# Kernel optimization log

Hardware: AMD Instinct MI355X
Metric: run time of the kernel (lower is better)

## Reference

```python
import jax, jax.numpy as jnp
import numpy as np

B, S, D = 4, 2048, 2048
NQ, NKV = 16, 4
HD = D // NQ          # head_size = 128
GROUP = NQ // NKV     # 4


def _rope_table(seq_len, head_size, theta=10000.0):
    # [seq, head_size/2, 2] = (cos, sin), matching torch polar freqs_cis
    inv = 1.0 / (theta ** (np.arange(0, head_size, 2, dtype=np.float32) / head_size))
    ang = np.arange(seq_len, dtype=np.float32)[:, None] * inv[None, :]
    return jnp.asarray(np.stack([np.cos(ang), np.sin(ang)], axis=-1))


def setup_inputs() -> dict:
    key = jax.random.key(0)
    ks = jax.random.split(key, 6)
    sd = 0.02
    return {
        "x": jax.random.normal(ks[0], (B, S, D), jnp.float32),
        "freq_cis": _rope_table(S, HD),
        "Wq": jax.random.normal(ks[1], (D, NQ * HD), jnp.float32) * sd,
        "bq": jnp.zeros((NQ * HD,), jnp.float32),
        "Wk": jax.random.normal(ks[2], (D, NKV * HD), jnp.float32) * sd,
        "bk": jnp.zeros((NKV * HD,), jnp.float32),
        "Wv": jax.random.normal(ks[3], (D, NKV * HD), jnp.float32) * sd,
        "bv": jnp.zeros((NKV * HD,), jnp.float32),
        "Wo": jax.random.normal(ks[4], (NQ * HD, D), jnp.float32) * sd,
        "start_pos": 0,
    }


def _apply_rope(x, fc):
    # x: [b, s, h, d]; fc: [s, d/2, 2] -> complex multiply on (even, odd) pairs
    xr = x.reshape(*x.shape[:-1], -1, 2)
    cos = fc[None, :, None, :, 0]
    sin = fc[None, :, None, :, 1]
    x0, x1 = xr[..., 0], xr[..., 1]
    out = jnp.stack([x0 * cos - x1 * sin, x0 * sin + x1 * cos], axis=-1)
    return out.reshape(x.shape)


def reference(x, freq_cis, Wq, bq, Wk, bk, Wv, bv, Wo, start_pos):
    b, s, _ = x.shape
    q = (x @ Wq + bq).reshape(b, s, NQ, HD)
    k = (x @ Wk + bk).reshape(b, s, NKV, HD)
    v = (x @ Wv + bv).reshape(b, s, NKV, HD)

    fc = freq_cis[start_pos:start_pos + s]
    q = _apply_rope(q, fc)
    k = _apply_rope(k, fc)

    # [b, nkv, group, s, d] query view; k/v stay [b, nkv, s, d] (GQA broadcast)
    q = q.transpose(0, 2, 1, 3).reshape(b, NKV, GROUP, s, HD)
    k = k.transpose(0, 2, 1, 3)
    v = v.transpose(0, 2, 1, 3)

    scale = 1.0 / jnp.sqrt(jnp.asarray(HD, x.dtype))
    scores = jnp.einsum("bhgqd,bhkd->bhgqk", q, k) * scale
    causal = jnp.tril(jnp.ones((s, s), bool))
    scores = jnp.where(causal[None, None, None], scores, jnp.asarray(-jnp.inf, scores.dtype))
    probs = jax.nn.softmax(scores, axis=-1)
    o = jnp.einsum("bhgqk,bhkd->bhgqd", probs, v)

    o = o.reshape(b, NQ, s, HD).transpose(0, 2, 1, 3).reshape(b, s, NQ * HD)
    return o @ Wo
```

## Files before the change

kernel.cpp:

```cpp
#include <hip/hip_runtime.h>
#include <stdint.h>

typedef __attribute__((ext_vector_type(8))) short bf16x8;
typedef __attribute__((ext_vector_type(4))) float f32x4;
typedef __attribute__((ext_vector_type(16))) float f32x16;

#define S_LEN 2048
#define D_MODEL 2048
#define NQH 16
#define NKVH 4
#define HDIM 128
#define BATCH 4

__device__ __forceinline__ float bf2f(unsigned short s) {
  union { unsigned u; float f; } v; v.u = ((unsigned)s) << 16; return v.f;
}
__device__ __forceinline__ unsigned short f2bf(float f) {
  union { float f; unsigned u; } v; v.f = f;
  unsigned r = v.u + 0x7FFFu + ((v.u >> 16) & 1u);
  return (unsigned short)(r >> 16);
}
__device__ __forceinline__ f32x4 fzero() {
  f32x4 v; v[0]=0.f; v[1]=0.f; v[2]=0.f; v[3]=0.f; return v;
}
__device__ __forceinline__ void async16(const void* g, void* l) {
  __builtin_amdgcn_global_load_lds(
      (const __attribute__((address_space(1))) unsigned int*)g,
      (__attribute__((address_space(3))) unsigned int*)l, 16, 0, 0);
}
__device__ __forceinline__ unsigned cvtpk(float lo, float hi) {
  unsigned r;
  asm("v_cvt_pk_bf16_f32 %0, %1, %2" : "=v"(r) : "v"(lo), "v"(hi));
  return r;
}

__global__ void k_convert_x(const float* __restrict__ x, unsigned short* __restrict__ xb, int n4) {
  int stride = gridDim.x * blockDim.x;
  for (int i = blockIdx.x * blockDim.x + threadIdx.x; i < n4; i += stride) {
    float4 v = ((const float4*)x)[i];
    ushort4 o;
    o.x = f2bf(v.x); o.y = f2bf(v.y); o.z = f2bf(v.z); o.w = f2bf(v.w);
    ((ushort4*)xb)[i] = o;
  }
}

__global__ void k_transpose_all(const float* __restrict__ Wq, const float* __restrict__ Wk,
                                const float* __restrict__ Wv, const float* __restrict__ Wo,
                                unsigned short* __restrict__ Wt, unsigned short* __restrict__ Wot) {
  __shared__ float tile[32][33];
  int bid = blockIdx.x;
  const float* W; unsigned short* D; int N, nx;
  if (bid < 4096)      { W = Wq; D = Wt;                          N = 2048; nx = 64; }
  else if (bid < 5120) { W = Wk; D = Wt + (size_t)2048 * 2048;    N = 512;  nx = 16; bid -= 4096; }
  else if (bid < 6144) { W = Wv; D = Wt + (size_t)2560 * 2048;    N = 512;  nx = 16; bid -= 5120; }
  else                 { W = Wo; D = Wot;                         N = 2048; nx = 64; bid -= 6144; }
  int tx = threadIdx.x & 31, ty = threadIdx.x >> 5;
  int n0 = (bid % nx) * 32, k0 = (bid / nx) * 32;
  #pragma unroll
  for (int i = 0; i < 4; ++i)
    tile[ty + i*8][tx] = W[(size_t)(k0 + ty + i*8) * N + n0 + tx];
  __syncthreads();
  #pragma unroll
  for (int i = 0; i < 4; ++i)
    D[(size_t)(n0 + ty + i*8) * 2048 + k0 + tx] = f2bf(tile[tx][ty + i*8]);
}

__global__ void k_ropeK(unsigned short* __restrict__ Kb, const float* __restrict__ fc,
                        const int* __restrict__ start_pos, int total) {
  int sp = start_pos[0];
  int stride = gridDim.x * blockDim.x;
  for (int i = blockIdx.x * blockDim.x + threadIdx.x; i < total; i += stride) {
    int d2 = i & 63;
    int s = (i >> 6) & (S_LEN - 1);
    unsigned v = ((unsigned*)Kb)[i];
    float x0 = bf2f((unsigned short)(v & 0xFFFFu));
    float x1 = bf2f((unsigned short)(v >> 16));
    float c  = fc[((size_t)(sp + s) * 64 + d2) * 2];
    float sn = fc[((size_t)(sp + s) * 64 + d2) * 2 + 1];
    float y0 = x0 * c - x1 * sn;
    float y1 = x0 * sn + x1 * c;
    ((unsigned*)Kb)[i] = (unsigned)f2bf(y0) | ((unsigned)f2bf(y1) << 16);
  }
}

#define BARRIER() __builtin_amdgcn_s_barrier()
#define LGKM0()  do { asm volatile("s_waitcnt lgkmcnt(0)" ::: "memory"); \
                      __builtin_amdgcn_sched_barrier(0); } while (0)
#define VMCNT6() asm volatile("s_waitcnt vmcnt(6)" ::: "memory")
#define VMCNT4() asm volatile("s_waitcnt vmcnt(4)" ::: "memory")
#define VMCNT0() asm volatile("s_waitcnt vmcnt(0)" ::: "memory")

__device__ __forceinline__ bf16x8 ldsrd(const unsigned short* L, int row, int kk, int g) {
  int Xs = (kk * 64 + g * 16) ^ ((row & 7) << 4);
  return *(const bf16x8*)&L[row * 64 + (Xs >> 1)];
}
__device__ __forceinline__ void stage8(const unsigned short* __restrict__ G, int gbase,
                                       int k0, unsigned short* lds, int rowbase, int lane) {
  int row = rowbase + (lane >> 3);
  int col8 = (lane & 7) ^ ((lane >> 3) & 7);
  async16(G + (size_t)(gbase + row) * 2048 + k0 + col8 * 8, lds + rowbase * 64 + lane * 8);
}

const float SCL2E_H = 0.08838834764831845f * 1.4426950408889634f;

__global__ __launch_bounds__(512, 2) void k_gemm_q(
    const unsigned short* __restrict__ A, const unsigned short* __restrict__ Bt,
    const float* __restrict__ bq, unsigned short* __restrict__ Qo)
{
  __shared__ __align__(16) unsigned short Abuf[2][256 * 64];
  __shared__ __align__(16) unsigned short Bbuf[2][256 * 64];
  const int NT = 32, NXT = 8;
  const int tid = threadIdx.x, lane = tid & 63, w = tid >> 6;
  const int lr = lane & 15, g = lane >> 4;
  const int wm = w >> 2, wn = w & 3;

  int nwg = NXT * 32;
  int cpx = nwg >> 3;
  int bid = blockIdx.x;
  int swz = (bid & 7) * cpx + (bid >> 3);
  const int by = swz / NXT, bx = swz % NXT;
  const int mbase = by * 256, nbase = bx * 256;

  #define ST_AQ02(tt) if ((tt) < NT) { unsigned short* L = Abuf[(tt) & 1]; int k0 = (tt) * 64; \
    _Pragma("unroll") for (int it = 0; it < 2; ++it) { int sub = it * 8 + w; \
      stage8(A, mbase, k0, L, (sub >> 3) * 128 + (sub & 7) * 8, lane); } }
  #define ST_AQ13(tt) if ((tt) < NT) { unsigned short* L = Abuf[(tt) & 1]; int k0 = (tt) * 64; \
    _Pragma("unroll") for (int it = 0; it < 2; ++it) { int sub = it * 8 + w; \
      stage8(A, mbase, k0, L, 64 + (sub >> 3) * 128 + (sub & 7) * 8, lane); } }
  #define ST_BS0(tt) if ((tt) < NT) { unsigned short* L = Bbuf[(tt) & 1]; int k0 = (tt) * 64; \
    _Pragma("unroll") for (int it = 0; it < 2; ++it) { int sub = it * 8 + w; \
      stage8(Bt, nbase, k0, L, (sub >> 2) * 64 + (sub & 3) * 8, lane); } }
  #define ST_BS1(tt) if ((tt) < NT) { unsigned short* L = Bbuf[(tt) & 1]; int k0 = (tt) * 64; \
    _Pragma("unroll") for (int it = 0; it < 2; ++it) { int sub = it * 8 + w; \
      stage8(Bt, nbase, k0, L, 32 + (sub >> 2) * 64 + (sub & 3) * 8, lane); } }

  f32x4 acc[8][4];
  #pragma unroll
  for (int m = 0; m < 8; ++m)
    #pragma unroll
    for (int n = 0; n < 4; ++n) acc[m][n] = fzero();

  ST_AQ02(0); ST_AQ13(0); ST_BS0(0); ST_BS1(0);
  ST_AQ02(1); ST_BS1(1);
  VMCNT4();
  BARRIER();

  bf16x8 a[2][4], b[2][2];

  for (int t = 0; t < NT; ++t) {
    const unsigned short* Al = Abuf[t & 1];
    const unsigned short* Bl = Bbuf[t & 1];

    #pragma unroll
    for (int kk = 0; kk < 2; ++kk) {
      #pragma unroll
      for (int m = 0; m < 4; ++m) a[kk][m] = ldsrd(Al, wm * 128 + m * 16 + lr, kk, g);
      #pragma unroll
      for (int n = 0; n < 2; ++n) b[kk][n] = ldsrd(Bl, wn * 64 + n * 16 + lr, kk, g);
    }
    ST_AQ13(t + 1);
    BARRIER(); LGKM0();
    __builtin_amdgcn_s_setprio(1);
    #pragma unroll
    for (int kk = 0; kk < 2; ++kk)
      #pragma unroll
      for (int m = 0; m < 4; ++m)
        #pragma unroll
        for (int n = 0; n < 2; ++n)
          acc[m][n] = __builtin_amdgcn_mfma_f32_16x16x32_bf16(a[kk][m], b[kk][n], acc[m][n], 0, 0, 0);
    __builtin_amdgcn_s_setprio(0);
    BARRIER();

    #pragma unroll
    for (int kk = 0; kk < 2; ++kk)
      #pragma unroll
      for (int n = 0; n < 2; ++n) b[kk][n] = ldsrd(Bl, wn * 64 + (2 + n) * 16 + lr, kk, g);
    ST_BS0(t + 1);
    BARRIER(); LGKM0();
    __builtin_amdgcn_s_setprio(1);
    #pragma unroll
    for (int kk = 0; kk < 2; ++kk)
      #pragma unroll
      for (int m = 0; m < 4; ++m)
        #pragma unroll
        for (int n = 0; n < 2; ++n)
          acc[m][2 + n] = __builtin_amdgcn_mfma_f32_16x16x32_bf16(a[kk][m], b[kk][n], acc[m][2 + n], 0, 0, 0);
    __builtin_amdgcn_s_setprio(0);
    BARRIER();

    #pragma unroll
    for (int kk = 0; kk < 2; ++kk)
      #pragma unroll
      for (int m = 0; m < 4; ++m) a[kk][m] = ldsrd(Al, wm * 128 + 64 + m * 16 + lr, kk, g);
    ST_AQ02(t + 2);
    BARRIER(); LGKM0();
    __builtin_amdgcn_s_setprio(1);
    #pragma unroll
    for (int kk = 0; kk < 2; ++kk)
      #pragma unroll
      for (int m = 0; m < 4; ++m)
        #pragma unroll
        for (int n = 0; n < 2; ++n)
          acc[4 + m][2 + n] = __builtin_amdgcn_mfma_f32_16x16x32_bf16(a[kk][m], b[kk][n], acc[4 + m][2 + n], 0, 0, 0);
    __builtin_amdgcn_s_setprio(0);
    BARRIER();

    #pragma unroll
    for (int kk = 0; kk < 2; ++kk)
      #pragma unroll
      for (int n = 0; n < 2; ++n) b[kk][n] = ldsrd(Bl, wn * 64 + n * 16 + lr, kk, g);
    ST_BS1(t + 2);
    VMCNT4();
    BARRIER(); LGKM0();
    __builtin_amdgcn_s_setprio(1);
    #pragma unroll
    for (int kk = 0; kk < 2; ++kk)
      #pragma unroll
      for (int m = 0; m < 4; ++m)
        #pragma unroll
        for (int n = 0; n < 2; ++n)
          acc[4 + m][n] = __builtin_amdgcn_mfma_f32_16x16x32_bf16(a[kk][m], b[kk][n], acc[4 + m][n], 0, 0, 0);
    __builtin_amdgcn_s_setprio(0);
    BARRIER();
  }

  #pragma unroll
  for (int n = 0; n < 4; ++n) {
    const int ng = nbase + wn * 64 + n * 16 + lr;
    const int hh = ng >> 7, dd = ng & 127;
    const float bias = bq[ng];
    #pragma unroll
    for (int m = 0; m < 8; ++m)
      #pragma unroll
      for (int i = 0; i < 4; ++i) {
        int mg = mbase + wm * 128 + m * 16 + g * 4 + i;
        int bb = mg >> 11, s = mg & 2047;
        float val = (acc[m][n][i] + bias) * SCL2E_H;
        Qo[((size_t)(bb * NQH + hh) * S_LEN + s) * HDIM + dd] = f2bf(val);
      }
  }
  #undef ST_AQ02
  #undef ST_AQ13
  #undef ST_BS0
  #undef ST_BS1
}

__global__ __launch_bounds__(512, 2) void k_gemm_kv(
    const unsigned short* __restrict__ A, const unsigned short* __restrict__ Bt,
    const float* __restrict__ bk, const float* __restrict__ bv,
    unsigned short* __restrict__ Ko, unsigned short* __restrict__ Vto)
{
  __shared__ __align__(16) unsigned short Ab[3][256 * 64];
  __shared__ __align__(16) unsigned short Bb[3][128 * 64];
  const int NT = 32, NXT = 8;
  const int tid = threadIdx.x, lane = tid & 63, w = tid >> 6;
  const int lr = lane & 15, g = lane >> 4;
  const int wm = w >> 1, wn = w & 1;

  int nwg = NXT * 32;
  int cpx = nwg >> 3;
  int bid = blockIdx.x;
  int swz = (bid & 7) * cpx + (bid >> 3);
  const int by = swz / NXT, bx = swz % NXT;
  const int mbase = by * 256, nbase = bx * 128;

  #define ST_A(tt) { unsigned short* L = Ab[(tt) % 3]; int k0 = (tt) * 64; \
    _Pragma("unroll") for (int it = 0; it < 4; ++it) { int c = tid + it * 512; \
      int row = c >> 3, col8 = (c & 7) ^ (row & 7); \
      async16(A + (size_t)(mbase + row) * 2048 + k0 + col8 * 8, L + c * 8); } }
  #define ST_B(tt) { unsigned short* L = Bb[(tt) % 3]; int k0 = (tt) * 64; \
    _Pragma("unroll") for (int it = 0; it < 2; ++it) { int c = tid + it * 512; \
      int row = c >> 3, col8 = (c & 7) ^ (row & 7); \
      async16(Bt + (size_t)(nbase + row) * 2048 + k0 + col8 * 8, L + c * 8); } }

  f32x4 acc[4][4];
  #pragma unroll
  for (int m = 0; m < 4; ++m)
    #pragma unroll
    for (int n = 0; n < 4; ++n) acc[m][n] = fzero();

  ST_A(0); ST_B(0); ST_A(1); ST_B(1);
  VMCNT6();
  BARRIER();

  for (int t = 0; t < NT; ++t) {
    const unsigned short* Al = Ab[t % 3];
    const unsigned short* Bl = Bb[t % 3];
    bf16x8 a[2][4], b[2][2];

    #pragma unroll
    for (int kk = 0; kk < 2; ++kk) {
      #pragma unroll
      for (int m = 0; m < 4; ++m) a[kk][m] = ldsrd(Al, wm * 64 + m * 16 + lr, kk, g);
      #pragma unroll
      for (int n = 0; n < 2; ++n) b[kk][n] = ldsrd(Bl, wn * 64 + n * 16 + lr, kk, g);
    }
    if (t + 2 < NT) ST_A(t + 2);
    BARRIER(); LGKM0();
    __builtin_amdgcn_s_setprio(1);
    #pragma unroll
    for (int kk = 0; kk < 2; ++kk)
      #pragma unroll
      for (int m = 0; m < 4; ++m)
        #pragma unroll
        for (int n = 0; n < 2; ++n)
          acc[m][n] = __builtin_amdgcn_mfma_f32_16x16x32_bf16(a[kk][m], b[kk][n], acc[m][n], 0, 0, 0);
    __builtin_amdgcn_s_setprio(0);
    BARRIER();

    #pragma unroll
    for (int kk = 0; kk < 2; ++kk)
      #pragma unroll
      for (int n = 0; n < 2; ++n) b[kk][n] = ldsrd(Bl, wn * 64 + (2 + n) * 16 + lr, kk, g);
    if (t + 2 < NT) { ST_B(t + 2); VMCNT6(); } else { VMCNT0(); }
    BARRIER(); LGKM0();
    __builtin_amdgcn_s_setprio(1);
    #pragma unroll
    for (int kk = 0; kk < 2; ++kk)
      #pragma unroll
      for (int m = 0; m < 4; ++m)
        #pragma unroll
        for (int n = 0; n < 2; ++n)
          acc[m][2 + n] = __builtin_amdgcn_mfma_f32_16x16x32_bf16(a[kk][m], b[kk][n], acc[m][2 + n], 0, 0, 0);
    __builtin_amdgcn_s_setprio(0);
    BARRIER();
  }

  #pragma unroll
  for (int n = 0; n < 4; ++n) {
    const int ng = nbase + wn * 64 + n * 16 + lr;
    const bool isK = (ng < 512);
    const int nn = isK ? ng : ng - 512;
    const int hh = nn >> 7, dd = nn & 127;
    const float bias = isK ? bk[nn] : bv[nn];
    #pragma unroll
    for (int m = 0; m < 4; ++m)
      #pragma unroll
      for (int i = 0; i < 4; ++i) {
        int mg = mbase + wm * 64 + m * 16 + g * 4 + i;
        int bb = mg >> 11, s = mg & 2047;
        float val = acc[m][n][i] + bias;
        if (isK) {
          Ko[((size_t)(bb * NKVH + hh) * S_LEN + s) * HDIM + dd] = f2bf(val);
        } else {
          Vto[((size_t)(bb * NKVH + hh) * HDIM + dd) * S_LEN + s] = f2bf(val);
        }
      }
  }
  #undef ST_A
  #undef ST_B
}

__global__ __launch_bounds__(512, 2) void k_gemm_out256(
    const unsigned short* __restrict__ A, const unsigned short* __restrict__ Bt,
    float* __restrict__ Cf)
{
  __shared__ __align__(16) unsigned short Abuf[2][256 * 64];
  __shared__ __align__(16) unsigned short Bbuf[2][256 * 64];
  const int NT = 32, NXT = 8;
  const int tid = threadIdx.x, lane = tid & 63, w = tid >> 6;
  const int lr = lane & 15, g = lane >> 4;
  const int wm = w >> 2, wn = w & 3;

  int nwg = NXT * 32;
  int cpx = nwg >> 3;
  int bid = blockIdx.x;
  int swz = (bid & 7) * cpx + (bid >> 3);
  const int by = swz / NXT, bx = swz % NXT;
  const int mbase = by * 256, nbase = bx * 256;

  #define ST_AQ02(tt) if ((tt) < NT) { unsigned short* L = Abuf[(tt) & 1]; int k0 = (tt) * 64; \
    _Pragma("unroll") for (int it = 0; it < 2; ++it) { int sub = it * 8 + w; \
      stage8(A, mbase, k0, L, (sub >> 3) * 128 + (sub & 7) * 8, lane); } }
  #define ST_AQ13(tt) if ((tt) < NT) { unsigned short* L = Abuf[(tt) & 1]; int k0 = (tt) * 64; \
    _Pragma("unroll") for (int it = 0; it < 2; ++it) { int sub = it * 8 + w; \
      stage8(A, mbase, k0, L, 64 + (sub >> 3) * 128 + (sub & 7) * 8, lane); } }
  #define ST_BS0(tt) if ((tt) < NT) { unsigned short* L = Bbuf[(tt) & 1]; int k0 = (tt) * 64; \
    _Pragma("unroll") for (int it = 0; it < 2; ++it) { int sub = it * 8 + w; \
      stage8(Bt, nbase, k0, L, (sub >> 2) * 64 + (sub & 3) * 8, lane); } }
  #define ST_BS1(tt) if ((tt) < NT) { unsigned short* L = Bbuf[(tt) & 1]; int k0 = (tt) * 64; \
    _Pragma("unroll") for (int it = 0; it < 2; ++it) { int sub = it * 8 + w; \
      stage8(Bt, nbase, k0, L, 32 + (sub >> 2) * 64 + (sub & 3) * 8, lane); } }

  f32x4 acc[8][4];
  #pragma unroll
  for (int m = 0; m < 8; ++m)
    #pragma unroll
    for (int n = 0; n < 4; ++n) acc[m][n] = fzero();

  ST_AQ02(0); ST_AQ13(0); ST_BS0(0); ST_BS1(0);
  ST_AQ02(1); ST_BS1(1);
  VMCNT4();
  BARRIER();

  bf16x8 a[2][4], b[2][2];

  for (int t = 0; t < NT; ++t) {
    const unsigned short* Al = Abuf[t & 1];
    const unsigned short* Bl = Bbuf[t & 1];

    #pragma unroll
    for (int kk = 0; kk < 2; ++kk) {
      #pragma unroll
      for (int m = 0; m < 4; ++m) a[kk][m] = ldsrd(Al, wm * 128 + m * 16 + lr, kk, g);
      #pragma unroll
      for (int n = 0; n < 2; ++n) b[kk][n] = ldsrd(Bl, wn * 64 + n * 16 + lr, kk, g);
    }
    ST_AQ13(t + 1);
    BARRIER(); LGKM0();
    __builtin_amdgcn_s_setprio(1);
    #pragma unroll
    for (int kk = 0; kk < 2; ++kk)
      #pragma unroll
      for (int m = 0; m < 4; ++m)
        #pragma unroll
        for (int n = 0; n < 2; ++n)
          acc[m][n] = __builtin_amdgcn_mfma_f32_16x16x32_bf16(a[kk][m], b[kk][n], acc[m][n], 0, 0, 0);
    __builtin_amdgcn_s_setprio(0);
    BARRIER();

    #pragma unroll
    for (int kk = 0; kk < 2; ++kk)
      #pragma unroll
      for (int n = 0; n < 2; ++n) b[kk][n] = ldsrd(Bl, wn * 64 + (2 + n) * 16 + lr, kk, g);
    ST_BS0(t + 1);
    BARRIER(); LGKM0();
    __builtin_amdgcn_s_setprio(1);
    #pragma unroll
    for (int kk = 0; kk < 2; ++kk)
      #pragma unroll
      for (int m = 0; m < 4; ++m)
        #pragma unroll
        for (int n = 0; n < 2; ++n)
          acc[m][2 + n] = __builtin_amdgcn_mfma_f32_16x16x32_bf16(a[kk][m], b[kk][n], acc[m][2 + n], 0, 0, 0);
    __builtin_amdgcn_s_setprio(0);
    BARRIER();

    #pragma unroll
    for (int kk = 0; kk < 2; ++kk)
      #pragma unroll
      for (int m = 0; m < 4; ++m) a[kk][m] = ldsrd(Al, wm * 128 + 64 + m * 16 + lr, kk, g);
    ST_AQ02(t + 2);
    BARRIER(); LGKM0();
    __builtin_amdgcn_s_setprio(1);
    #pragma unroll
    for (int kk = 0; kk < 2; ++kk)
      #pragma unroll
      for (int m = 0; m < 4; ++m)
        #pragma unroll
        for (int n = 0; n < 2; ++n)
          acc[4 + m][2 + n] = __builtin_amdgcn_mfma_f32_16x16x32_bf16(a[kk][m], b[kk][n], acc[4 + m][2 + n], 0, 0, 0);
    __builtin_amdgcn_s_setprio(0);
    BARRIER();

    #pragma unroll
    for (int kk = 0; kk < 2; ++kk)
      #pragma unroll
      for (int n = 0; n < 2; ++n) b[kk][n] = ldsrd(Bl, wn * 64 + n * 16 + lr, kk, g);
    ST_BS1(t + 2);
    VMCNT4();
    BARRIER(); LGKM0();
    __builtin_amdgcn_s_setprio(1);
    #pragma unroll
    for (int kk = 0; kk < 2; ++kk)
      #pragma unroll
      for (int m = 0; m < 4; ++m)
        #pragma unroll
        for (int n = 0; n < 2; ++n)
          acc[4 + m][n] = __builtin_amdgcn_mfma_f32_16x16x32_bf16(a[kk][m], b[kk][n], acc[4 + m][n], 0, 0, 0);
    __builtin_amdgcn_s_setprio(0);
    BARRIER();
  }

  #pragma unroll
  for (int m = 0; m < 8; ++m)
    #pragma unroll
    for (int n = 0; n < 4; ++n)
      #pragma unroll
      for (int i = 0; i < 4; ++i) {
        int mg = mbase + wm * 128 + m * 16 + g * 4 + i;
        int ng = nbase + wn * 64 + n * 16 + lr;
        Cf[(size_t)mg * 2048 + ng] = acc[m][n][i];
      }
  #undef ST_AQ02
  #undef ST_AQ13
  #undef ST_BS0
  #undef ST_BS1
}

__global__ __launch_bounds__(256, 2) void k_flash2(
    const unsigned short* __restrict__ Q, const unsigned short* __restrict__ K,
    const unsigned short* __restrict__ Vt, unsigned short* __restrict__ O,
    const float* __restrict__ fc, const int* __restrict__ start_pos)
{
  __shared__ __align__(16) unsigned short SH[32768];

  const int tid = threadIdx.x;
  const int lane = tid & 63;
  const int w = tid >> 6;
  const int ql = lane & 31;
  const int hi = lane >> 5;

  const int bh = blockIdx.x >> 3;
  const int tp = blockIdx.x & 7;
  const int b = bh >> 4, h = bh & 15;
  const int kh = h >> 2;
  const int sp = start_pos[0];

  const unsigned short* Qbase = Q + (size_t)(b * NQH + h) * S_LEN * HDIM;
  const unsigned short* Kbase = K + (size_t)(b * NKVH + kh) * S_LEN * HDIM;
  const unsigned short* Vtb   = Vt + (size_t)(b * NKVH + kh) * HDIM * S_LEN;

  #define STAGEKV(jj) { unsigned short* Kd = SH + ((jj) & 1) * 16384; \
    unsigned short* Vd = Kd + 8192; \
    _Pragma("unroll") for (int it = 0; it < 4; ++it) { \
      int c = tid + it * 256; int row = c >> 4, col = c & 15; \
      int lcol = col ^ (row & 15); \
      async16(Kbase + (size_t)((jj) * 64 + row) * HDIM + lcol * 8, Kd + c * 8); } \
    _Pragma("unroll") for (int it = 0; it < 4; ++it) { \
      int c = tid + it * 256; int row = c >> 3, col = c & 7; \
      int lcol = col ^ (row & 7); \
      async16(Vtb + (size_t)row * S_LEN + (jj) * 64 + lcol * 8, Vd + c * 8); } }

  #pragma unroll 1
  for (int half = 0; half < 2; ++half) {
    const int t = half ? (15 - tp) : tp;
    const int nkv = 2 * t + 2;
    const int qg = t * 128 + w * 32 + ql;

    __syncthreads();

    bf16x8 qf[8];
    {
      const unsigned short* qp = Qbase + (size_t)qg * HDIM;
      const float* fcrow = fc + (size_t)(sp + qg) * 128;
      #pragma unroll
      for (int dd = 0; dd < 8; ++dd) {
        bf16x8 raw = *(const bf16x8*)(qp + dd * 16 + hi * 8);
        int d2b = (dd * 16 + hi * 8) >> 1;
        union { unsigned u[4]; bf16x8 v; } out;
        #pragma unroll
        for (int u2 = 0; u2 < 4; ++u2) {
          float x0 = bf2f((unsigned short)raw[2 * u2]);
          float x1 = bf2f((unsigned short)raw[2 * u2 + 1]);
          float2 cs = *(const float2*)&fcrow[(d2b + u2) * 2];
          out.u[u2] = cvtpk(x0 * cs.x - x1 * cs.y, x0 * cs.y + x1 * cs.x);
        }
        qf[dd] = out.v;
      }
    }

    float m_r = -1e30f, l_r = 0.f;
    f32x16 oA[4];
    #pragma unroll
    for (int db = 0; db < 4; ++db)
      #pragma unroll
      for (int r = 0; r < 16; ++r) oA[db][r] = 0.f;

    STAGEKV(0);
    __syncthreads();

    for (int j = 0; j < nkv; ++j) {
      const unsigned short* Kl = SH + (j & 1) * 16384;
      const unsigned short* Vl = Kl + 8192;

      if (j + 1 < nkv) STAGEKV(j + 1);

      if (j * 64 <= t * 128 + w * 32 + 31) {
        f32x16 p0, p1;
        #pragma unroll
        for (int r = 0; r < 16; ++r) { p0[r] = 0.f; p1[r] = 0.f; }
        __builtin_amdgcn_s_setprio(1);
        #pragma unroll
        for (int dd = 0; dd < 8; ++dd) {
          const int off = (((dd * 32 + hi * 16) ^ ((ql & 15) << 4)) >> 1);
          bf16x8 a0 = *(const bf16x8*)&Kl[ql * 128 + off];
          bf16x8 a1 = *(const bf16x8*)&Kl[(32 + ql) * 128 + off];
          p0 = __builtin_amdgcn_mfma_f32_32x32x16_bf16(a0, qf[dd], p0, 0, 0, 0);
          p1 = __builtin_amdgcn_mfma_f32_32x32x16_bf16(a1, qf[dd], p1, 0, 0, 0);
        }
        __builtin_amdgcn_s_setprio(0);

        #pragma unroll
        for (int r = 0; r < 16; ++r) {
          const int kl = (r & 3) + 8 * (r >> 2);
          int kg = j * 64 + kl + 4 * hi;
          if (kg > qg) p0[r] = -1e30f;
          if (kg + 32 > qg) p1[r] = -1e30f;
        }

        float pm = -1e30f;
        #pragma unroll
        for (int r = 0; r < 16; ++r) pm = fmaxf(pm, fmaxf(p0[r], p1[r]));
        pm = fmaxf(pm, __shfl_xor(pm, 32));
        if (!__all(pm - m_r <= 8.0f)) {
          const float mn = fmaxf(m_r, pm);
          const float corr = exp2f(m_r - mn);
          m_r = mn;
          l_r *= corr;
          #pragma unroll
          for (int db = 0; db < 4; ++db)
            #pragma unroll
            for (int r = 0; r < 16; ++r) oA[db][r] *= corr;
        }
        float rs = 0.f;
        #pragma unroll
        for (int r = 0; r < 16; ++r) {
          p0[r] = exp2f(p0[r] - m_r);
          p1[r] = exp2f(p1[r] - m_r);
          rs += p0[r] + p1[r];
        }
        rs += __shfl_xor(rs, 32);
        l_r += rs;

        bf16x8 pb[4];
        {
          unsigned Wv[8], W2v[8];
          #pragma unroll
          for (int d = 0; d < 4; ++d) {
            Wv[d]      = cvtpk(p0[4*d],     p0[4*d + 1]);
            W2v[d]     = cvtpk(p0[4*d + 2], p0[4*d + 3]);
            Wv[4 + d]  = cvtpk(p1[4*d],     p1[4*d + 1]);
            W2v[4 + d] = cvtpk(p1[4*d + 2], p1[4*d + 3]);
          }
          #pragma unroll
          for (int kt = 0; kt < 2; ++kt) {
            #pragma unroll
            for (int s = 0; s < 2; ++s) {
              unsigned ownW   = hi ? Wv[kt*4 + 2*s + 1]  : Wv[kt*4 + 2*s];
              unsigned sendW  = hi ? Wv[kt*4 + 2*s]      : Wv[kt*4 + 2*s + 1];
              unsigned recvW  = (unsigned)__shfl_xor((int)sendW, 32);
              unsigned ownW2  = hi ? W2v[kt*4 + 2*s + 1] : W2v[kt*4 + 2*s];
              unsigned sendW2 = hi ? W2v[kt*4 + 2*s]     : W2v[kt*4 + 2*s + 1];
              unsigned recvW2 = (unsigned)__shfl_xor((int)sendW2, 32);
              union { unsigned u[4]; bf16x8 v; } pk;
              pk.u[0] = hi ? recvW  : ownW;
              pk.u[1] = hi ? recvW2 : ownW2;
              pk.u[2] = hi ? ownW   : recvW;
              pk.u[3] = hi ? ownW2  : recvW2;
              pb[kt*2 + s] = pk.v;
            }
          }
        }

        __builtin_amdgcn_s_setprio(1);
        #pragma unroll
        for (int ks = 0; ks < 4; ++ks) {
          #pragma unroll
          for (int db = 0; db < 4; ++db) {
            const int off = (((ks * 32 + hi * 16) ^ ((ql & 7) << 4)) >> 1);
            bf16x8 av = *(const bf16x8*)&Vl[(db * 32 + ql) * 64 + off];
            oA[db] = __builtin_amdgcn_mfma_f32_32x32x16_bf16(av, pb[ks], oA[db], 0, 0, 0);
          }
        }
        __builtin_amdgcn_s_setprio(0);
      }
      __syncthreads();
    }

    {
      const float invl = 1.f / l_r;
      const int qloc = w * 32 + ql;
      #pragma unroll
      for (int db = 0; db < 4; ++db)
        #pragma unroll
        for (int g4 = 0; g4 < 4; ++g4) {
          unsigned lo  = cvtpk(oA[db][g4*4 + 0] * invl, oA[db][g4*4 + 1] * invl);
          unsigned hi2 = cvtpk(oA[db][g4*4 + 2] * invl, oA[db][g4*4 + 3] * invl);
          int byteoff = qloc * 256 + ((db * 64 + g4 * 16 + hi * 8) ^ ((qloc & 7) << 4));
          *(uint2*)((char*)SH + byteoff) = make_uint2(lo, hi2);
        }
    }
    __syncthreads();
    {
      const int q2 = tid >> 1, hf = tid & 1;
      unsigned short* orow = O + ((size_t)(b * S_LEN + t * 128 + q2)) * D_MODEL + h * HDIM + hf * 64;
      #pragma unroll
      for (int u = 0; u < 8; ++u) {
        int byteoff = q2 * 256 + ((hf * 128 + u * 16) ^ ((q2 & 7) << 4));
        bf16x8 v = *(const bf16x8*)((const char*)SH + byteoff);
        *(bf16x8*)(orow + u * 8) = v;
      }
    }
  }
  #undef STAGEKV
}

extern "C" void kernel_launch(void* const* d_in, const int* in_sizes, int n_in,
                              void* d_out, int out_size, void* d_ws, size_t ws_size,
                              hipStream_t stream) {
  (void)in_sizes; (void)n_in; (void)out_size; (void)ws_size;
  const float* x  = (const float*)d_in[0];
  const float* fc = (const float*)d_in[1];
  const float* Wq = (const float*)d_in[2];
  const float* bq = (const float*)d_in[3];
  const float* Wk = (const float*)d_in[4];
  const float* bk = (const float*)d_in[5];
  const float* Wv = (const float*)d_in[6];
  const float* bv = (const float*)d_in[7];
  const float* Wo = (const float*)d_in[8];
  const int* start_pos = (const int*)d_in[9];
  float* out = (float*)d_out;

  unsigned short* ws = (unsigned short*)d_ws;
  size_t off = 0;
  unsigned short* xb  = ws + off; off += (size_t)8192 * 2048;
  unsigned short* Wt  = ws + off; off += (size_t)3072 * 2048;
  unsigned short* Wot = ws + off; off += (size_t)2048 * 2048;
  unsigned short* Qb  = ws + off; off += (size_t)BATCH * NQH  * S_LEN * HDIM;
  unsigned short* Kb  = ws + off; off += (size_t)BATCH * NKVH * S_LEN * HDIM;
  unsigned short* Vtb = ws + off; off += (size_t)BATCH * NKVH * S_LEN * HDIM;
  unsigned short* Ob  = ws + off; off += (size_t)8192 * 2048;

  k_convert_x<<<2048, 256, 0, stream>>>(x, xb, 8192 * 2048 / 4);
  k_transpose_all<<<10240, 256, 0, stream>>>(Wq, Wk, Wv, Wo, Wt, Wot);

  k_gemm_q<<<dim3(256), 512, 0, stream>>>(xb, Wt, bq, Qb);
  k_gemm_kv<<<dim3(256), 512, 0, stream>>>(xb, Wt + (size_t)2048 * 2048, bk, bv, Kb, Vtb);

  k_ropeK<<<512, 256, 0, stream>>>(Kb, fc, start_pos, BATCH * NKVH * S_LEN * 64);

  k_flash2<<<dim3(512), 256, 0, stream>>>(Qb, Kb, Vtb, Ob, fc, start_pos);

  k_gemm_out256<<<dim3(256), 512, 0, stream>>>(Ob, Wot, out);
}
```

Before: 362.6 us.

## Shrink flash attention KV tile to 32 and launch one block per query tile

The attention kernel now stages 32-key K/V tiles instead of 64, which halves shared memory and raises launch bounds to 4 blocks per CU. It drops the paired-tile (t, 15-t) load balancing and launches 1024 blocks, one per 128-query tile. The causal mask is applied only on the diagonal tile per wave, and tile skipping is done at 32-key granularity. The cost is more loop iterations and barriers, lower MFMA work per sync, and load balance that now relies on the hardware scheduler instead of explicit pairing.

```diff
diff --git a/kernel.cpp b/kernel.cpp
--- a/kernel.cpp
+++ b/kernel.cpp
@@ -488,12 +488,12 @@
   #undef ST_BS1
 }
 
-__global__ __launch_bounds__(256, 2) void k_flash2(
+__global__ __launch_bounds__(256, 4) void k_flash2(
     const unsigned short* __restrict__ Q, const unsigned short* __restrict__ K,
     const unsigned short* __restrict__ Vt, unsigned short* __restrict__ O,
     const float* __restrict__ fc, const int* __restrict__ start_pos)
 {
-  __shared__ __align__(16) unsigned short SH[32768];
+  __shared__ __align__(16) unsigned short SH[16384];
 
   const int tid = threadIdx.x;
   const int lane = tid & 63;
@@ -501,8 +501,8 @@
   const int ql = lane & 31;
   const int hi = lane >> 5;
 
-  const int bh = blockIdx.x >> 3;
-  const int tp = blockIdx.x & 7;
+  const int bh = blockIdx.x >> 4;
+  const int t  = blockIdx.x & 15;
   const int b = bh >> 4, h = bh & 15;
   const int kh = h >> 2;
   const int sp = start_pos[0];
@@ -511,176 +511,163 @@
   const unsigned short* Kbase = K + (size_t)(b * NKVH + kh) * S_LEN * HDIM;
   const unsigned short* Vtb   = Vt + (size_t)(b * NKVH + kh) * HDIM * S_LEN;
 
-  #define STAGEKV(jj) { unsigned short* Kd = SH + ((jj) & 1) * 16384; \
-    unsigned short* Vd = Kd + 8192; \
-    _Pragma("unroll") for (int it = 0; it < 4; ++it) { \
+  #define STAGEKV(jj) { unsigned short* Kd = SH + ((jj) & 1) * 8192; \
+    unsigned short* Vd = Kd + 4096; \
+    _Pragma("unroll") for (int it = 0; it < 2; ++it) { \
       int c = tid + it * 256; int row = c >> 4, col = c & 15; \
-      int lcol = col ^ (row & 15); \
-      async16(Kbase + (size_t)((jj) * 64 + row) * HDIM + lcol * 8, Kd + c * 8); } \
-    _Pragma("unroll") for (int it = 0; it < 4; ++it) { \
-      int c = tid + it * 256; int row = c >> 3, col = c & 7; \
-      int lcol = col ^ (row & 7); \
-      async16(Vtb + (size_t)row * S_LEN + (jj) * 64 + lcol * 8, Vd + c * 8); } }
-
-  #pragma unroll 1
-  for (int half = 0; half < 2; ++half) {
-    const int t = half ? (15 - tp) : tp;
-    const int nkv = 2 * t + 2;
-    const int qg = t * 128 + w * 32 + ql;
-
-    __syncthreads();
-
-    bf16x8 qf[8];
-    {
-      const unsigned short* qp = Qbase + (size_t)qg * HDIM;
-      const float* fcrow = fc + (size_t)(sp + qg) * 128;
+      int lcol = (col & 8) | ((col ^ (row & 7)) & 7); \
+      async16(Kbase + (size_t)((jj) * 32 + row) * HDIM + lcol * 8, Kd + c * 8); } \
+    _Pragma("unroll") for (int it = 0; it < 2; ++it) { \
+      int c = tid + it * 256; int row = c >> 2, col = c & 3; \
+      int lcol = col ^ (row & 3); \
+      async16(Vtb + (size_t)row * S_LEN + (jj) * 32 + lcol * 8, Vd + c * 8); } }
+
+  const int nkv = 4 * t + 4;
+  const int qg = t * 128 + w * 32 + ql;
+  const int jd = 4 * t + w;
+
+  bf16x8 qf[8];
+  {
+    const unsigned short* qp = Qbase + (size_t)qg * HDIM;
+    const float* fcrow = fc + (size_t)(sp + qg) * 128;
+    #pragma unroll
+    for (int dd = 0; dd < 8; ++dd) {
+      bf16x8 raw = *(const bf16x8*)(qp + dd * 16 + hi * 8);
+      int d2b = (dd * 16 + hi * 8) >> 1;
+      union { unsigned u[4]; bf16x8 v; } out;
+      #pragma unroll
+      for (int u2 = 0; u2 < 4; ++u2) {
+        float x0 = bf2f((unsigned short)raw[2 * u2]);
+        float x1 = bf2f((unsigned short)raw[2 * u2 + 1]);
+        float2 cs = *(const float2*)&fcrow[(d2b + u2) * 2];
+        out.u[u2] = cvtpk(x0 * cs.x - x1 * cs.y, x0 * cs.y + x1 * cs.x);
+      }
+      qf[dd] = out.v;
+    }
+  }
+
+  float m_r = -1e30f, l_r = 0.f;
+  f32x16 oA[4];
+  #pragma unroll
+  for (int db = 0; db < 4; ++db)
+    #pragma unroll
+    for (int r = 0; r < 16; ++r) oA[db][r] = 0.f;
+
+  STAGEKV(0);
+  __syncthreads();
+
+  for (int j = 0; j < nkv; ++j) {
+    const unsigned short* Kl = SH + (j & 1) * 8192;
+    const unsigned short* Vl = Kl + 4096;
+
+    if (j + 1 < nkv) STAGEKV(j + 1);
+
+    if (j <= jd) {
+      f32x16 p0;
+      #pragma unroll
+      for (int r = 0; r < 16; ++r) p0[r] = 0.f;
+      __builtin_amdgcn_s_setprio(1);
       #pragma unroll
       for (int dd = 0; dd < 8; ++dd) {
-        bf16x8 raw = *(const bf16x8*)(qp + dd * 16 + hi * 8);
-        int d2b = (dd * 16 + hi * 8) >> 1;
-        union { unsigned u[4]; bf16x8 v; } out;
-        #pragma unroll
-        for (int u2 = 0; u2 < 4; ++u2) {
-          float x0 = bf2f((unsigned short)raw[2 * u2]);
-          float x1 = bf2f((unsigned short)raw[2 * u2 + 1]);
-          float2 cs = *(const float2*)&fcrow[(d2b + u2) * 2];
-          out.u[u2] = cvtpk(x0 * cs.x - x1 * cs.y, x0 * cs.y + x1 * cs.x);
+        const int off = (((dd * 32 + hi * 16) ^ ((ql & 7) << 4)) >> 1);
+        bf16x8 a0 = *(const bf16x8*)&Kl[ql * 128 + off];
+        p0 = __builtin_amdgcn_mfma_f32_32x32x16_bf16(a0, qf[dd], p0, 0, 0, 0);
+      }
+      __builtin_amdgcn_s_setprio(0);
+
+      if (j == jd) {
+        #pragma unroll
+        for (int r = 0; r < 16; ++r) {
+          const int kl = (r & 3) + 8 * (r >> 2) + 4 * hi;
+          if (kl > ql) p0[r] = -1e30f;
         }
-        qf[dd] = out.v;
-      }
-    }
-
-    float m_r = -1e30f, l_r = 0.f;
-    f32x16 oA[4];
-    #pragma unroll
-    for (int db = 0; db < 4; ++db)
-      #pragma unroll
-      for (int r = 0; r < 16; ++r) oA[db][r] = 0.f;
-
-    STAGEKV(0);
-    __syncthreads();
-
-    for (int j = 0; j < nkv; ++j) {
-      const unsigned short* Kl = SH + (j & 1) * 16384;
-      const unsigned short* Vl = Kl + 8192;
-
-      if (j + 1 < nkv) STAGEKV(j + 1);
-
-      if (j * 64 <= t * 128 + w * 32 + 31) {
-        f32x16 p0, p1;
-        #pragma unroll
-        for (int r = 0; r < 16; ++r) { p0[r] = 0.f; p1[r] = 0.f; }
-        __builtin_amdgcn_s_setprio(1);
-        #pragma unroll
-        for (int dd = 0; dd < 8; ++dd) {
-          const int off = (((dd * 32 + hi * 16) ^ ((ql & 15) << 4)) >> 1);
-          bf16x8 a0 = *(const bf16x8*)&Kl[ql * 128 + off];
-          bf16x8 a1 = *(const bf16x8*)&Kl[(32 + ql) * 128 + off];
-          p0 = __builtin_amdgcn_mfma_f32_32x32x16_bf16(a0, qf[dd], p0, 0, 0, 0);
-          p1 = __builtin_amdgcn_mfma_f32_32x32x16_bf16(a1, qf[dd], p1, 0, 0, 0);
+      }
+
+      float pm = -1e30f;
+      #pragma unroll
+      for (int r = 0; r < 16; ++r) pm = fmaxf(pm, p0[r]);
+      pm = fmaxf(pm, __shfl_xor(pm, 32));
+      if (!__all(pm - m_r <= 8.0f)) {
+        const float mn = fmaxf(m_r, pm);
+        const float corr = exp2f(m_r - mn);
+        m_r = mn;
+        l_r *= corr;
+        #pragma unroll
+        for (int db = 0; db < 4; ++db)
+          #pragma unroll
+          for (int r = 0; r < 16; ++r) oA[db][r] *= corr;
+      }
+      float rs = 0.f;
+      #pragma unroll
+      for (int r = 0; r < 16; ++r) {
+        p0[r] = exp2f(p0[r] - m_r);
+        rs += p0[r];
+      }
+      rs += __shfl_xor(rs, 32);
+      l_r += rs;
+
+      bf16x8 pb[2];
+      {
+        unsigned Wv[4], W2v[4];
+        #pragma unroll
+        for (int d = 0; d < 4; ++d) {
+          Wv[d]  = cvtpk(p0[4*d],     p0[4*d + 1]);
+          W2v[d] = cvtpk(p0[4*d + 2], p0[4*d + 3]);
         }
-        __builtin_amdgcn_s_setprio(0);
-
-        #pragma unroll
-        for (int r = 0; r < 16; ++r) {
-          const int kl = (r & 3) + 8 * (r >> 2);
-          int kg = j * 64 + kl + 4 * hi;
-          if (kg > qg) p0[r] = -1e30f;
-          if (kg + 32 > qg) p1[r] = -1e30f;
+        #pragma unroll
+        for (int s = 0; s < 2; ++s) {
+          unsigned ownW   = hi ? Wv[2*s + 1]  : Wv[2*s];
+          unsigned sendW  = hi ? Wv[2*s]      : Wv[2*s + 1];
+          unsigned recvW  = (unsigned)__shfl_xor((int)sendW, 32);
+          unsigned ownW2  = hi ? W2v[2*s + 1] : W2v[2*s];
+          unsigned sendW2 = hi ? W2v[2*s]     : W2v[2*s + 1];
+          unsigned recvW2 = (unsigned)__shfl_xor((int)sendW2, 32);
+          union { unsigned u[4]; bf16x8 v; } pk;
+          pk.u[0] = hi ? recvW  : ownW;
+          pk.u[1] = hi ? recvW2 : ownW2;
+          pk.u[2] = hi ? ownW   : recvW;
+          pk.u[3] = hi ? ownW2  : recvW2;
+          pb[s] = pk.v;
         }
-
-        float pm = -1e30f;
-        #pragma unroll
-        for (int r = 0; r < 16; ++r) pm = fmaxf(pm, fmaxf(p0[r], p1[r]));
-        pm = fmaxf(pm, __shfl_xor(pm, 32));
-        if (!__all(pm - m_r <= 8.0f)) {
-          const float mn = fmaxf(m_r, pm);
-          const float corr = exp2f(m_r - mn);
-          m_r = mn;
-          l_r *= corr;
-          #pragma unroll
-          for (int db = 0; db < 4; ++db)
-            #pragma unroll
-            for (int r = 0; r < 16; ++r) oA[db][r] *= corr;
+      }
+
+      __builtin_amdgcn_s_setprio(1);
+      #pragma unroll
+      for (int ks = 0; ks < 2; ++ks) {
+        #pragma unroll
+        for (int db = 0; db < 4; ++db) {
+          const int off = (((ks * 32 + hi * 16) ^ ((ql & 3) << 4)) >> 1);
+          bf16x8 av = *(const bf16x8*)&Vl[(db * 32 + ql) * 32 + off];
+          oA[db] = __builtin_amdgcn_mfma_f32_32x32x16_bf16(av, pb[ks], oA[db], 0, 0, 0);
         }
-        float rs = 0.f;
-        #pragma unroll
-        for (int r = 0; r < 16; ++r) {
-          p0[r] = exp2f(p0[r] - m_r);
-          p1[r] = exp2f(p1[r] - m_r);
-          rs += p0[r] + p1[r];
-        }
-        rs += __shfl_xor(rs, 32);
-        l_r += rs;
-
-        bf16x8 pb[4];
-        {
-          unsigned Wv[8], W2v[8];
-          #pragma unroll
-          for (int d = 0; d < 4; ++d) {
-            Wv[d]      = cvtpk(p0[4*d],     p0[4*d + 1]);
-            W2v[d]     = cvtpk(p0[4*d + 2], p0[4*d + 3]);
-            Wv[4 + d]  = cvtpk(p1[4*d],     p1[4*d + 1]);
-            W2v[4 + d] = cvtpk(p1[4*d + 2], p1[4*d + 3]);
-          }
-          #pragma unroll
-          for (int kt = 0; kt < 2; ++kt) {
-            #pragma unroll
-            for (int s = 0; s < 2; ++s) {
-              unsigned ownW   = hi ? Wv[kt*4 + 2*s + 1]  : Wv[kt*4 + 2*s];
-              unsigned sendW  = hi ? Wv[kt*4 + 2*s]      : Wv[kt*4 + 2*s + 1];
-              unsigned recvW  = (unsigned)__shfl_xor((int)sendW, 32);
-              unsigned ownW2  = hi ? W2v[kt*4 + 2*s + 1] : W2v[kt*4 + 2*s];
-              unsigned sendW2 = hi ? W2v[kt*4 + 2*s]     : W2v[kt*4 + 2*s + 1];
-              unsigned recvW2 = (unsigned)__shfl_xor((int)sendW2, 32);
-              union { unsigned u[4]; bf16x8 v; } pk;
-              pk.u[0] = hi ? recvW  : ownW;
-              pk.u[1] = hi ? recvW2 : ownW2;
-              pk.u[2] = hi ? ownW   : recvW;
-              pk.u[3] = hi ? ownW2  : recvW2;
-              pb[kt*2 + s] = pk.v;
-            }
-          }
-        }
-
-        __builtin_amdgcn_s_setprio(1);
-        #pragma unroll
-        for (int ks = 0; ks < 4; ++ks) {
-          #pragma unroll
-          for (int db = 0; db < 4; ++db) {
-            const int off = (((ks * 32 + hi * 16) ^ ((ql & 7) << 4)) >> 1);
-            bf16x8 av = *(const bf16x8*)&Vl[(db * 32 + ql) * 64 + off];
-            oA[db] = __builtin_amdgcn_mfma_f32_32x32x16_bf16(av, pb[ks], oA[db], 0, 0, 0);
-          }
-        }
-        __builtin_amdgcn_s_setprio(0);
-      }
-      __syncthreads();
-    }
-
-    {
-      const float invl = 1.f / l_r;
-      const int qloc = w * 32 + ql;
-      #pragma unroll
-      for (int db = 0; db < 4; ++db)
-        #pragma unroll
-        for (int g4 = 0; g4 < 4; ++g4) {
-          unsigned lo  = cvtpk(oA[db][g4*4 + 0] * invl, oA[db][g4*4 + 1] * invl);
-          unsigned hi2 = cvtpk(oA[db][g4*4 + 2] * invl, oA[db][g4*4 + 3] * invl);
-          int byteoff = qloc * 256 + ((db * 64 + g4 * 16 + hi * 8) ^ ((qloc & 7) << 4));
-          *(uint2*)((char*)SH + byteoff) = make_uint2(lo, hi2);
-        }
+      }
+      __builtin_amdgcn_s_setprio(0);
     }
     __syncthreads();
-    {
-      const int q2 = tid >> 1, hf = tid & 1;
-      unsigned short* orow = O + ((size_t)(b * S_LEN + t * 128 + q2)) * D_MODEL + h * HDIM + hf * 64;
-      #pragma unroll
-      for (int u = 0; u < 8; ++u) {
-        int byteoff = q2 * 256 + ((hf * 128 + u * 16) ^ ((q2 & 7) << 4));
-        bf16x8 v = *(const bf16x8*)((const char*)SH + byteoff);
-        *(bf16x8*)(orow + u * 8) = v;
-      }
+  }
+
+  {
+    const float invl = 1.f / l_r;
+    const int qloc = w * 32 + ql;
+    #pragma unroll
+    for (int db = 0; db < 4; ++db)
+      #pragma unroll
+      for (int g4 = 0; g4 < 4; ++g4) {
+        unsigned lo  = cvtpk(oA[db][g4*4 + 0] * invl, oA[db][g4*4 + 1] * invl);
+        unsigned hi2 = cvtpk(oA[db][g4*4 + 2] * invl, oA[db][g4*4 + 3] * invl);
+        int byteoff = qloc * 256 + ((db * 64 + g4 * 16 + hi * 8) ^ ((qloc & 7) << 4));
+        *(uint2*)((char*)SH + byteoff) = make_uint2(lo, hi2);
+      }
+  }
+  __syncthreads();
+  {
+    const int q2 = tid >> 1, hf = tid & 1;
+    unsigned short* orow = O + ((size_t)(b * S_LEN + t * 128 + q2)) * D_MODEL + h * HDIM + hf * 64;
+    #pragma unroll
+    for (int u = 0; u < 8; ++u) {
+      int byteoff = q2 * 256 + ((hf * 128 + u * 16) ^ ((q2 & 7) << 4));
+      bf16x8 v = *(const bf16x8*)((const char*)SH + byteoff);
+      *(bf16x8*)(orow + u * 8) = v;
     }
   }
   #undef STAGEKV
@@ -720,7 +707,7 @@
 
   k_ropeK<<<512, 256, 0, stream>>>(Kb, fc, start_pos, BATCH * NKVH * S_LEN * 64);
 
-  k_flash2<<<dim3(512), 256, 0, stream>>>(Qb, Kb, Vtb, Ob, fc, start_pos);
+  k_flash2<<<dim3(1024), 256, 0, stream>>>(Qb, Kb, Vtb, Ob, fc, start_pos);
 
   k_gemm_out256<<<dim3(256), 512, 0, stream>>>(Ob, Wot, out);
 }
```

New measurement: 477.0 us. 1.32x slower.
